# Kernel tuning notes

Measured on AMD Instinct MI355X. Metric: run time of the kernel, lower is better.

## Reference

```python
import jax, jax.numpy as jnp
import numpy as np
from jax import lax

COUNT_W, DM_W, OT_W = 3.0, 0.5, 0.3
SL1_BETA = 10.0
DM_SIGMA, DM_DS = 8.0, 4
OT_REG, OT_ITERS, OT_DS = 0.1, 50, 8
EPS = 1e-8


def _gauss_kernel(sigma):
    size = int(6 * sigma) | 1  # 49
    x = np.arange(size, dtype=np.float32) - size // 2
    xx, yy = np.meshgrid(x, x)
    k = np.exp(-(xx ** 2 + yy ** 2) / (2 * sigma ** 2))
    k = k / k.sum()
    return jnp.asarray(k, jnp.float32)[None, None], size // 2  # [1,1,S,S], pad


def _block_sum(x, d):
    # avg_pool2d(kernel=d) * d^2 == block sum
    B, C, H, W = x.shape
    return x.reshape(B, C, H // d, d, W // d, d).sum(axis=(3, 5))


def _cost_matrix(H, W):
    y, x = jnp.meshgrid(jnp.arange(H, dtype=jnp.float32),
                        jnp.arange(W, dtype=jnp.float32), indexing='ij')
    coords = jnp.stack([y.ravel(), x.ravel()], axis=1)  # [N,2]
    d = coords[:, None, :] - coords[None, :, :]
    return (d ** 2).sum(-1)  # [N,N] squared euclidean


def _dm_loss(pred, gt):
    p = _block_sum(pred, DM_DS)
    g = _block_sum(gt, DM_DS)
    kern, pad = _gauss_kernel(DM_SIGMA)
    conv = lambda z: lax.conv_general_dilated(
        z, kern, (1, 1), [(pad, pad), (pad, pad)],
        dimension_numbers=('NCHW', 'OIHW', 'NCHW'))
    ps, gs = conv(p), conv(g)
    pn = ps / jnp.maximum(ps.sum(axis=(2, 3), keepdims=True), EPS)
    gn = gs / jnp.maximum(gs.sum(axis=(2, 3), keepdims=True), EPS)
    kl = (gn * jnp.log((gn + EPS) / (pn + EPS))).sum(axis=(2, 3))
    l2 = ((pn - gn) ** 2).sum(axis=(2, 3))
    return kl.mean() + l2.mean()


def _ot_loss(pred, gt):
    p = _block_sum(pred, OT_DS)  # [B,1,h,w]
    g = _block_sum(gt, OT_DS)
    B, _, h, w = p.shape
    N = h * w
    a_raw = p.reshape(B, N)
    b_raw = g.reshape(B, N)
    a_sum = jnp.maximum(a_raw.sum(-1), EPS)
    b_sum = jnp.maximum(b_raw.sum(-1), EPS)
    a = a_raw / a_sum[:, None]
    b = b_raw / b_sum[:, None]
    C = _cost_matrix(h, w)          # [N,N]
    K = jnp.exp(-C / OT_REG)        # [N,N]

    def step(uv, _):
        u, _v = uv
        v = b / (u @ K + EPS)       # K.T @ u, batched
        u = a / (v @ K.T + EPS)     # K @ v, batched
        return (u, v), None

    (u, v), _ = lax.scan(step, (jnp.ones_like(a), jnp.ones_like(b)),
                         None, length=OT_ITERS)
    cost = jnp.einsum('bn,nm,bm->b', u, K * C, v)  # sum(P*C), P=diag(u)K diag(v)
    mask = (a_sum > 0.5) & (b_sum > 0.5)
    return jnp.where(mask, cost, 0.0).sum() / B


def reference(pred_density, gt_density, gt_counts, cell_area):
    B = pred_density.shape[0]
    # count loss (smooth L1, beta=10)
    pred_counts = jnp.maximum(pred_density.sum(axis=(1, 2, 3)) / cell_area, 0.0)
    gt_counts_f = gt_counts.astype(jnp.float32)
    diff = jnp.abs(pred_counts - gt_counts_f)
    count_loss = jnp.where(diff < SL1_BETA,
                           0.5 * diff ** 2 / SL1_BETA,
                           diff - 0.5 * SL1_BETA).mean()
    dm = _dm_loss(pred_density, gt_density)
    ot = _ot_loss(pred_density, gt_density)
    return COUNT_W * count_loss + DM_W * dm + OT_W * ot


def setup_inputs() -> dict:
    key = jax.random.key(0)
    k1, k2, k3 = jax.random.split(key, 3)
    B, H, W = 16, 512, 512
    return {
        'pred_density': jax.random.uniform(k1, (B, 1, H, W), jnp.float32),
        'gt_density': jax.random.uniform(k2, (B, 1, H, W), jnp.float32),
        'gt_counts': jax.random.randint(k3, (B,), 0, 500, jnp.int32),
        'cell_area': 1,
    }
```

## Files before the change

### kernel.cpp

```cpp
#include <hip/hip_runtime.h>
#include <math.h>

constexpr int B   = 16;
constexpr int H   = 512, W = 512;
constexpr int HW  = H * W;
constexpr int P4  = 128;
constexpr int P4N = P4 * P4;
constexpr int P8N = 64 * 64;
constexpr int NIMG = 2 * B;

constexpr float KW1 = 4.5399929762484854e-05f;
constexpr float KC2 = 4.1223072448771156e-09f;

constexpr size_t OFF_P4   = 0;
constexpr size_t OFF_CV   = OFF_P4  + (size_t)NIMG * P4N;
constexpr size_t OFF_P8   = OFF_CV  + (size_t)NIMG * P4N;
constexpr size_t OFF_PART = OFF_P8  + (size_t)NIMG * P8N;
constexpr size_t OFF_CSUM = OFF_PART + 512;

__device__ __forceinline__ float dpp_up(float x) {
    return __int_as_float(__builtin_amdgcn_update_dpp(
        0, __float_as_int(x), 0x138, 0xf, 0xf, true));
}
__device__ __forceinline__ float dpp_dn(float x) {
    return __int_as_float(__builtin_amdgcn_update_dpp(
        0, __float_as_int(x), 0x130, 0xf, 0xf, true));
}

__global__ void k_pre8(const float* __restrict__ pred, const float* __restrict__ gt,
                       float* __restrict__ ws, float* __restrict__ out, int out_size) {
    int tid = threadIdx.x, bx = blockIdx.x;
    if (bx == 0) {
        for (int i = tid; i < out_size; i += 256) out[i] = 0.f;
    }
    int gid = bx * 256 + tid;
    int img = gid >> 12;
    int rem = gid & (P8N - 1);
    int y = rem >> 6, x = rem & 63;
    const float* src = (img < B) ? (pred + (size_t)img * HW)
                                 : (gt + (size_t)(img - B) * HW);
    const float4* s4 = reinterpret_cast<const float4*>(src);
    int base = y * 8 * 128 + x * 2;
    float q00 = 0.f, q01 = 0.f, q10 = 0.f, q11 = 0.f;
#pragma unroll
    for (int r = 0; r < 8; r++) {
        float4 a0 = s4[base + r * 128];
        float4 a1 = s4[base + r * 128 + 1];
        float sa = a0.x + a0.y + a0.z + a0.w;
        float sb = a1.x + a1.y + a1.z + a1.w;
        if (r < 4) { q00 += sa; q01 += sb; } else { q10 += sa; q11 += sb; }
    }
    float* p4 = ws + OFF_P4 + (size_t)img * P4N;
    p4[(2 * y) * 128 + 2 * x]       = q00;
    p4[(2 * y) * 128 + 2 * x + 1]   = q01;
    p4[(2 * y + 1) * 128 + 2 * x]   = q10;
    p4[(2 * y + 1) * 128 + 2 * x + 1] = q11;
    float s8 = q00 + q01 + q10 + q11;
    ws[OFF_P8 + gid] = s8;
    float part = s8;
#pragma unroll
    for (int o = 32; o > 0; o >>= 1) part += __shfl_down(part, o, 64);
    __shared__ float r4[4];
    int lane = tid & 63, wid = tid >> 6;
    if (lane == 0) r4[wid] = part;
    __syncthreads();
    if (tid == 0) ws[OFF_PART + bx] = r4[0] + r4[1] + r4[2] + r4[3];
}

__global__ void __launch_bounds__(1024) k_conv(float* __restrict__ ws) {
    __shared__ float hbuf[P4N];
    __shared__ float wlds[49];
    __shared__ float rs[16];
    int img = blockIdx.x, tid = threadIdx.x;
    if (tid < 49) {
        float xx = (float)(tid - 24);
        wlds[tid] = expf(-xx * xx * (1.f / 128.f));
    }
    __syncthreads();
    float norm = 0.f;
#pragma unroll
    for (int k = 0; k < 49; k++) norm += wlds[k];
    float inv = 1.f / norm;
    const float* src = ws + OFF_P4 + (size_t)img * P4N;

#pragma unroll
    for (int g = 0; g < 2; g++) {
        int unit = g * 1024 + tid;
        int r = unit >> 4, seg = unit & 15, x0 = seg * 8;
        const float4* row4 = reinterpret_cast<const float4*>(src + (size_t)r * 128);
        float v[56];
#pragma unroll
        for (int j = 0; j < 14; j++) {
            int fx = (x0 - 24) / 4 + j;
            float4 t = (fx >= 0 && fx < 32) ? row4[fx] : make_float4(0.f, 0.f, 0.f, 0.f);
            v[4 * j] = t.x; v[4 * j + 1] = t.y; v[4 * j + 2] = t.z; v[4 * j + 3] = t.w;
        }
        float o8[8];
#pragma unroll
        for (int i = 0; i < 8; i++) o8[i] = 0.f;
#pragma unroll
        for (int k = 0; k < 49; k++) {
            float wk = wlds[k];
#pragma unroll
            for (int i = 0; i < 8; i++) o8[i] = fmaf(wk, v[i + k], o8[i]);
        }
        int sw = r & 31;
#pragma unroll
        for (int i = 0; i < 8; i++)
            hbuf[r * 128 + ((x0 + i) ^ sw)] = o8[i] * inv;
    }
    __syncthreads();

    float part = 0.f;
    float* dst = ws + OFF_CV + (size_t)img * P4N;
#pragma unroll
    for (int g = 0; g < 2; g++) {
        int unit = g * 1024 + tid;
        int c = unit & 127, rseg = unit >> 7, r0 = rseg * 8;
        float v[56];
#pragma unroll
        for (int j = 0; j < 56; j++) {
            int rr = r0 - 24 + j;
            v[j] = (rr >= 0 && rr < 128) ? hbuf[rr * 128 + (c ^ (rr & 31))] : 0.f;
        }
        float o8[8];
#pragma unroll
        for (int i = 0; i < 8; i++) o8[i] = 0.f;
#pragma unroll
        for (int k = 0; k < 49; k++) {
            float wk = wlds[k];
#pragma unroll
            for (int i = 0; i < 8; i++) o8[i] = fmaf(wk, v[i + k], o8[i]);
        }
#pragma unroll
        for (int i = 0; i < 8; i++) {
            float s = o8[i] * inv;
            dst[(size_t)(r0 + i) * 128 + c] = s;
            part += s;
        }
    }
#pragma unroll
    for (int o = 32; o > 0; o >>= 1) part += __shfl_down(part, o, 64);
    int lane = tid & 63, wid = tid >> 6;
    if (lane == 0) rs[wid] = part;
    __syncthreads();
    if (tid == 0) {
        float s = 0.f;
#pragma unroll
        for (int i = 0; i < 16; i++) s += rs[i];
        ws[OFF_CSUM + img] = s;
    }
}

__global__ void k_kll2(const float* __restrict__ ws, float* __restrict__ out) {
    int idx = blockIdx.x * 256 + threadIdx.x;
    int b = idx >> 12, rem = idx & 4095;
    const float4* cv4 = reinterpret_cast<const float4*>(ws + OFF_CV);
    float4 p = cv4[(size_t)b * 4096 + rem];
    float4 g = cv4[(size_t)(B + b) * 4096 + rem];
    float isp = 1.f / fmaxf(ws[OFF_CSUM + b], 1e-8f);
    float isg = 1.f / fmaxf(ws[OFF_CSUM + B + b], 1e-8f);
    float part = 0.f;
#pragma unroll
    for (int j = 0; j < 4; j++) {
        float pn = (j == 0 ? p.x : j == 1 ? p.y : j == 2 ? p.z : p.w) * isp;
        float gn = (j == 0 ? g.x : j == 1 ? g.y : j == 2 ? g.z : g.w) * isg;
        float d = pn - gn;
        part += gn * __logf((gn + 1e-8f) / (pn + 1e-8f)) + d * d;
    }
#pragma unroll
    for (int o = 32; o > 0; o >>= 1) part += __shfl_down(part, o, 64);
    __shared__ float r4[4];
    int lane = threadIdx.x & 63, wid = threadIdx.x >> 6;
    if (lane == 0) r4[wid] = part;
    __syncthreads();
    if (threadIdx.x == 0)
        atomicAdd(out, (0.5f / 16.f) * (r4[0] + r4[1] + r4[2] + r4[3]));
}

__device__ __forceinline__ void matvec(float* cur, const float* tgt,
                                       float* hL, float* hR, int w, int lane) {
    hL[w * 64 + lane] = cur[0];
    hR[w * 64 + lane] = cur[7];
    __syncthreads();
    float lh = (w > 0) ? hR[(w - 1) * 64 + lane] : 0.f;
    float rh = (w < 7) ? hL[(w + 1) * 64 + lane] : 0.f;
    float t[8];
    t[0] = fmaf(KW1, lh + cur[1], cur[0]);
#pragma unroll
    for (int c = 1; c < 7; c++) t[c] = fmaf(KW1, cur[c - 1] + cur[c + 1], cur[c]);
    t[7] = fmaf(KW1, cur[6] + rh, cur[7]);
#pragma unroll
    for (int c = 0; c < 8; c++) {
        float s = fmaf(KW1, dpp_up(t[c]) + dpp_dn(t[c]), t[c]) + 1e-8f;
        cur[c] = tgt[c] * __builtin_amdgcn_rcpf(s);
    }
}

__global__ void __launch_bounds__(512) k_ot(const float* __restrict__ ws,
                                            const int* __restrict__ gtc,
                                            const int* __restrict__ carea,
                                            float* __restrict__ out) {
    __shared__ float smem[2 * 64 * 65];
    __shared__ float rsum[8];
    int b = blockIdx.x, tid = threadIdx.x;
    int lane = tid & 63;
    int w = tid >> 6;
    float* hL0 = smem;            float* hR0 = smem + 512;
    float* hL1 = smem + 1024;     float* hR1 = smem + 1536;

    const float* PART = ws + OFF_PART;
    float rawA = 0.f, rawB = 0.f;
#pragma unroll
    for (int j = 0; j < 16; j++) {
        rawA += PART[b * 16 + j];
        rawB += PART[(B + b) * 16 + j];
    }
    float asum = fmaxf(rawA, 1e-8f), bsum = fmaxf(rawB, 1e-8f);
    float ai = 1.f / asum, bi = 1.f / bsum;

    const float* ap = ws + OFF_P8 + (size_t)b * P8N;
    const float* bp = ws + OFF_P8 + (size_t)(B + b) * P8N;
    for (int i = tid; i < P8N; i += 512) {
        int r = i >> 6, c = i & 63;
        smem[r * 65 + c] = ap[i];
        smem[64 * 65 + r * 65 + c] = bp[i];
    }
    __syncthreads();
    float ar[8], br[8], cur[8], vv[8];
    int gc = w * 8;
#pragma unroll
    for (int c = 0; c < 8; c++) {
        ar[c] = smem[lane * 65 + gc + c] * ai;
        br[c] = smem[64 * 65 + lane * 65 + gc + c] * bi;
        cur[c] = 1.f;
    }
    __syncthreads();

    for (int it = 0; it < 50; it++) {
        matvec(cur, br, hL0, hR0, w, lane);
        if (it == 49) {
#pragma unroll
            for (int c = 0; c < 8; c++) vv[c] = cur[c];
        }
        matvec(cur, ar, hL1, hR1, w, lane);
    }

    hL0[w * 64 + lane] = vv[0];
    hR0[w * 64 + lane] = vv[7];
    __syncthreads();
    float V[10];
    V[0] = (w > 0) ? hR0[(w - 1) * 64 + lane] : 0.f;
    V[9] = (w < 7) ? hL0[(w + 1) * 64 + lane] : 0.f;
#pragma unroll
    for (int c = 0; c < 8; c++) V[c + 1] = vv[c];
    float U[10], D[10];
#pragma unroll
    for (int i = 0; i < 10; i++) { U[i] = dpp_up(V[i]); D[i] = dpp_dn(V[i]); }
    float part = 0.f;
#pragma unroll
    for (int c = 0; c < 8; c++) {
        float s = KW1 * (V[c] + V[c + 2] + U[c + 1] + D[c + 1])
                + KC2 * (U[c] + D[c] + U[c + 2] + D[c + 2]);
        part += cur[c] * s;
    }
#pragma unroll
    for (int o = 32; o > 0; o >>= 1) part += __shfl_down(part, o, 64);
    if (lane == 0) rsum[w] = part;
    __syncthreads();
    if (tid == 0) {
        float c = 0.f;
#pragma unroll
        for (int i = 0; i < 8; i++) c += rsum[i];
        float ot = (asum > 0.5f && bsum > 0.5f) ? c : 0.f;
        int cv = carea[0];
        float ca = (cv >= 1 && cv < 16777216) ? (float)cv : __int_as_float(cv);
        float pc = fmaxf(rawA / ca, 0.f);
        float d = fabsf(pc - (float)gtc[b]);
        float cl = (d < 10.f) ? (0.05f * d * d) : (d - 5.f);
        atomicAdd(out, 0.3f * ot * (1.f / 16.f) + 3.f * cl * (1.f / 16.f));
    }
}

extern "C" void kernel_launch(void* const* d_in, const int* in_sizes, int n_in,
                              void* d_out, int out_size, void* d_ws, size_t ws_size,
                              hipStream_t stream) {
    const float* pred = (const float*)d_in[0];
    const float* gt   = (const float*)d_in[1];
    const int* gtc    = (const int*)d_in[2];
    const int* ca     = (const int*)d_in[3];
    float* out = (float*)d_out;
    float* ws  = (float*)d_ws;

    k_pre8<<<512, 256, 0, stream>>>(pred, gt, ws, out, out_size);
    k_conv<<<32, 1024, 0, stream>>>(ws);
    k_kll2<<<256, 256, 0, stream>>>(ws, out);
    k_ot<<<16, 512, 0, stream>>>(ws, gtc, ca, out);
}
```

Before: 137.5 us.

## Merge conv and OT Sinkhorn into one launch running on disjoint blocks

Folds the separable Gaussian conv kernel and the OT Sinkhorn kernel into a single 48-block launch: 32 blocks do the conv at 512 threads and 16 blocks run Sinkhorn. The two stages run concurrently and one launch is dropped. The Sinkhorn layout changes from column strips to row strips read straight from global memory. Each iteration now computes v with halo rows, so it needs one barrier per iteration instead of two, using double-buffered halos. The conv blocks now have half the threads, each doing twice the work, which may lengthen the conv phase.

After: 123.8 us. 10.0% less time.

```diff
diff --git a/kernel.cpp b/kernel.cpp
--- a/kernel.cpp
+++ b/kernel.cpp
@@ -51,9 +51,9 @@
         if (r < 4) { q00 += sa; q01 += sb; } else { q10 += sa; q11 += sb; }
     }
     float* p4 = ws + OFF_P4 + (size_t)img * P4N;
-    p4[(2 * y) * 128 + 2 * x]       = q00;
-    p4[(2 * y) * 128 + 2 * x + 1]   = q01;
-    p4[(2 * y + 1) * 128 + 2 * x]   = q10;
+    p4[(2 * y) * 128 + 2 * x]         = q00;
+    p4[(2 * y) * 128 + 2 * x + 1]     = q01;
+    p4[(2 * y + 1) * 128 + 2 * x]     = q10;
     p4[(2 * y + 1) * 128 + 2 * x + 1] = q11;
     float s8 = q00 + q01 + q10 + q11;
     ws[OFF_P8 + gid] = s8;
@@ -67,88 +67,188 @@
     if (tid == 0) ws[OFF_PART + bx] = r4[0] + r4[1] + r4[2] + r4[3];
 }
 
-__global__ void __launch_bounds__(1024) k_conv(float* __restrict__ ws) {
-    __shared__ float hbuf[P4N];
-    __shared__ float wlds[49];
-    __shared__ float rs[16];
-    int img = blockIdx.x, tid = threadIdx.x;
-    if (tid < 49) {
-        float xx = (float)(tid - 24);
-        wlds[tid] = expf(-xx * xx * (1.f / 128.f));
-    }
-    __syncthreads();
-    float norm = 0.f;
-#pragma unroll
-    for (int k = 0; k < 49; k++) norm += wlds[k];
-    float inv = 1.f / norm;
-    const float* src = ws + OFF_P4 + (size_t)img * P4N;
-
-#pragma unroll
-    for (int g = 0; g < 2; g++) {
-        int unit = g * 1024 + tid;
-        int r = unit >> 4, seg = unit & 15, x0 = seg * 8;
-        const float4* row4 = reinterpret_cast<const float4*>(src + (size_t)r * 128);
-        float v[56];
-#pragma unroll
-        for (int j = 0; j < 14; j++) {
-            int fx = (x0 - 24) / 4 + j;
-            float4 t = (fx >= 0 && fx < 32) ? row4[fx] : make_float4(0.f, 0.f, 0.f, 0.f);
-            v[4 * j] = t.x; v[4 * j + 1] = t.y; v[4 * j + 2] = t.z; v[4 * j + 3] = t.w;
-        }
-        float o8[8];
-#pragma unroll
-        for (int i = 0; i < 8; i++) o8[i] = 0.f;
-#pragma unroll
-        for (int k = 0; k < 49; k++) {
-            float wk = wlds[k];
-#pragma unroll
-            for (int i = 0; i < 8; i++) o8[i] = fmaf(wk, v[i + k], o8[i]);
-        }
-        int sw = r & 31;
-#pragma unroll
-        for (int i = 0; i < 8; i++)
-            hbuf[r * 128 + ((x0 + i) ^ sw)] = o8[i] * inv;
-    }
-    __syncthreads();
-
-    float part = 0.f;
-    float* dst = ws + OFF_CV + (size_t)img * P4N;
-#pragma unroll
-    for (int g = 0; g < 2; g++) {
-        int unit = g * 1024 + tid;
-        int c = unit & 127, rseg = unit >> 7, r0 = rseg * 8;
-        float v[56];
-#pragma unroll
-        for (int j = 0; j < 56; j++) {
-            int rr = r0 - 24 + j;
-            v[j] = (rr >= 0 && rr < 128) ? hbuf[rr * 128 + (c ^ (rr & 31))] : 0.f;
-        }
-        float o8[8];
-#pragma unroll
-        for (int i = 0; i < 8; i++) o8[i] = 0.f;
-#pragma unroll
-        for (int k = 0; k < 49; k++) {
-            float wk = wlds[k];
-#pragma unroll
-            for (int i = 0; i < 8; i++) o8[i] = fmaf(wk, v[i + k], o8[i]);
-        }
-#pragma unroll
-        for (int i = 0; i < 8; i++) {
-            float s = o8[i] * inv;
-            dst[(size_t)(r0 + i) * 128 + c] = s;
-            part += s;
-        }
-    }
-#pragma unroll
-    for (int o = 32; o > 0; o >>= 1) part += __shfl_down(part, o, 64);
-    int lane = tid & 63, wid = tid >> 6;
-    if (lane == 0) rs[wid] = part;
-    __syncthreads();
-    if (tid == 0) {
-        float s = 0.f;
-#pragma unroll
-        for (int i = 0; i < 16; i++) s += rs[i];
-        ws[OFF_CSUM + img] = s;
+__global__ void __launch_bounds__(512) k_mega(float* __restrict__ ws,
+                                              const int* __restrict__ gtc,
+                                              const int* __restrict__ carea,
+                                              float* __restrict__ out) {
+    __shared__ float sh[P4N + 80];
+    int tid = threadIdx.x;
+    int lane = tid & 63, w = tid >> 6;
+
+    if (blockIdx.x < 32) {
+        int img = blockIdx.x;
+        float* hbuf = sh;
+        float* wlds = sh + P4N;
+        float* rs   = sh + P4N + 56;
+        if (tid < 49) {
+            float xx = (float)(tid - 24);
+            wlds[tid] = expf(-xx * xx * (1.f / 128.f));
+        }
+        __syncthreads();
+        float norm = 0.f;
+#pragma unroll
+        for (int k = 0; k < 49; k++) norm += wlds[k];
+        float inv = 1.f / norm;
+        const float* src = ws + OFF_P4 + (size_t)img * P4N;
+
+#pragma unroll
+        for (int g = 0; g < 4; g++) {
+            int unit = g * 512 + tid;
+            int r = unit >> 4, seg = unit & 15, x0 = seg * 8;
+            const float4* row4 = reinterpret_cast<const float4*>(src + (size_t)r * 128);
+            float v[56];
+#pragma unroll
+            for (int j = 0; j < 14; j++) {
+                int fx = (x0 - 24) / 4 + j;
+                float4 t = (fx >= 0 && fx < 32) ? row4[fx] : make_float4(0.f, 0.f, 0.f, 0.f);
+                v[4 * j] = t.x; v[4 * j + 1] = t.y; v[4 * j + 2] = t.z; v[4 * j + 3] = t.w;
+            }
+            float o8[8];
+#pragma unroll
+            for (int i = 0; i < 8; i++) o8[i] = 0.f;
+#pragma unroll
+            for (int k = 0; k < 49; k++) {
+                float wk = wlds[k];
+#pragma unroll
+                for (int i = 0; i < 8; i++) o8[i] = fmaf(wk, v[i + k], o8[i]);
+            }
+            int sw = r & 31;
+#pragma unroll
+            for (int i = 0; i < 8; i++)
+                hbuf[r * 128 + ((x0 + i) ^ sw)] = o8[i] * inv;
+        }
+        __syncthreads();
+
+        float part = 0.f;
+        float* dst = ws + OFF_CV + (size_t)img * P4N;
+#pragma unroll
+        for (int g = 0; g < 4; g++) {
+            int unit = g * 512 + tid;
+            int c = unit & 127, rseg = unit >> 7, r0 = rseg * 8;
+            float v[56];
+#pragma unroll
+            for (int j = 0; j < 56; j++) {
+                int rr = r0 - 24 + j;
+                v[j] = (rr >= 0 && rr < 128) ? hbuf[rr * 128 + (c ^ (rr & 31))] : 0.f;
+            }
+            float o8[8];
+#pragma unroll
+            for (int i = 0; i < 8; i++) o8[i] = 0.f;
+#pragma unroll
+            for (int k = 0; k < 49; k++) {
+                float wk = wlds[k];
+#pragma unroll
+                for (int i = 0; i < 8; i++) o8[i] = fmaf(wk, v[i + k], o8[i]);
+            }
+#pragma unroll
+            for (int i = 0; i < 8; i++) {
+                float s = o8[i] * inv;
+                dst[(size_t)(r0 + i) * 128 + c] = s;
+                part += s;
+            }
+        }
+#pragma unroll
+        for (int o = 32; o > 0; o >>= 1) part += __shfl_down(part, o, 64);
+        if (lane == 0) rs[w] = part;
+        __syncthreads();
+        if (tid == 0) {
+            float s = 0.f;
+#pragma unroll
+            for (int i = 0; i < 8; i++) s += rs[i];
+            ws[OFF_CSUM + img] = s;
+        }
+    } else {
+        int b = blockIdx.x - 32;
+        int r0 = w << 3;
+        float* H0 = sh;
+        float* H1 = sh + 2048;
+        float* rsum = sh + 4096;
+
+        const float* PART = ws + OFF_PART;
+        float rawA = 0.f, rawB = 0.f;
+#pragma unroll
+        for (int j = 0; j < 16; j++) {
+            rawA += PART[b * 16 + j];
+            rawB += PART[(B + b) * 16 + j];
+        }
+        float asum = fmaxf(rawA, 1e-8f), bsum = fmaxf(rawB, 1e-8f);
+        float ai = 1.f / asum, bi = 1.f / bsum;
+        const float* ap = ws + OFF_P8 + (size_t)b * P8N;
+        const float* bp = ws + OFF_P8 + (size_t)(B + b) * P8N;
+
+        float ar[8], br10[10], cur[8], vr[10];
+#pragma unroll
+        for (int k = 0; k < 8; k++) {
+            ar[k] = ap[(r0 + k) * 64 + lane] * ai;
+            cur[k] = 1.f;
+        }
+#pragma unroll
+        for (int i = 0; i < 10; i++) {
+            int rr = r0 - 1 + i;
+            br10[i] = (rr >= 0 && rr < 64) ? bp[rr * 64 + lane] * bi : 0.f;
+        }
+
+        for (int it = 0; it < 50; it++) {
+            float* Hp = (it & 1) ? H1 : H0;
+            Hp[(0 * 8 + w) * 64 + lane] = cur[0];
+            Hp[(1 * 8 + w) * 64 + lane] = cur[1];
+            Hp[(2 * 8 + w) * 64 + lane] = cur[6];
+            Hp[(3 * 8 + w) * 64 + lane] = cur[7];
+            __syncthreads();
+            float uext[12];
+            uext[0]  = w ? Hp[(2 * 8 + w - 1) * 64 + lane] : 0.f;
+            uext[1]  = w ? Hp[(3 * 8 + w - 1) * 64 + lane] : 0.f;
+#pragma unroll
+            for (int k = 0; k < 8; k++) uext[2 + k] = cur[k];
+            uext[10] = (w < 7) ? Hp[(0 * 8 + w + 1) * 64 + lane] : 0.f;
+            uext[11] = (w < 7) ? Hp[(1 * 8 + w + 1) * 64 + lane] : 0.f;
+
+            float tr[10];
+#pragma unroll
+            for (int i = 0; i < 10; i++)
+                tr[i] = fmaf(KW1, uext[i] + uext[i + 2], uext[i + 1]);
+#pragma unroll
+            for (int i = 0; i < 10; i++) {
+                float s = fmaf(KW1, dpp_up(tr[i]) + dpp_dn(tr[i]), tr[i]) + 1e-8f;
+                vr[i] = br10[i] * __builtin_amdgcn_rcpf(s);
+            }
+            float t2[8];
+#pragma unroll
+            for (int k = 0; k < 8; k++)
+                t2[k] = fmaf(KW1, vr[k] + vr[k + 2], vr[k + 1]);
+#pragma unroll
+            for (int k = 0; k < 8; k++) {
+                float s = fmaf(KW1, dpp_up(t2[k]) + dpp_dn(t2[k]), t2[k]) + 1e-8f;
+                cur[k] = ar[k] * __builtin_amdgcn_rcpf(s);
+            }
+        }
+
+        float dL[10], dR[10];
+#pragma unroll
+        for (int i = 0; i < 10; i++) { dL[i] = dpp_up(vr[i]); dR[i] = dpp_dn(vr[i]); }
+        float part = 0.f;
+#pragma unroll
+        for (int k = 0; k < 8; k++) {
+            float s = KW1 * (vr[k] + vr[k + 2] + dL[k + 1] + dR[k + 1])
+                    + KC2 * (dL[k] + dR[k] + dL[k + 2] + dR[k + 2]);
+            part = fmaf(cur[k], s, part);
+        }
+#pragma unroll
+        for (int o = 32; o > 0; o >>= 1) part += __shfl_down(part, o, 64);
+        if (lane == 0) rsum[w] = part;
+        __syncthreads();
+        if (tid == 0) {
+            float c = 0.f;
+#pragma unroll
+            for (int i = 0; i < 8; i++) c += rsum[i];
+            float ot = (asum > 0.5f && bsum > 0.5f) ? c : 0.f;
+            int cv = carea[0];
+            float ca = (cv >= 1 && cv < 16777216) ? (float)cv : __int_as_float(cv);
+            float pc = fmaxf(rawA / ca, 0.f);
+            float d = fabsf(pc - (float)gtc[b]);
+            float cl = (d < 10.f) ? (0.05f * d * d) : (d - 5.f);
+            atomicAdd(out, 0.3f * ot * (1.f / 16.f) + 3.f * cl * (1.f / 16.f));
+        }
     }
 }
 
@@ -178,110 +278,6 @@
         atomicAdd(out, (0.5f / 16.f) * (r4[0] + r4[1] + r4[2] + r4[3]));
 }
 
-__device__ __forceinline__ void matvec(float* cur, const float* tgt,
-                                       float* hL, float* hR, int w, int lane) {
-    hL[w * 64 + lane] = cur[0];
-    hR[w * 64 + lane] = cur[7];
-    __syncthreads();
-    float lh = (w > 0) ? hR[(w - 1) * 64 + lane] : 0.f;
-    float rh = (w < 7) ? hL[(w + 1) * 64 + lane] : 0.f;
-    float t[8];
-    t[0] = fmaf(KW1, lh + cur[1], cur[0]);
-#pragma unroll
-    for (int c = 1; c < 7; c++) t[c] = fmaf(KW1, cur[c - 1] + cur[c + 1], cur[c]);
-    t[7] = fmaf(KW1, cur[6] + rh, cur[7]);
-#pragma unroll
-    for (int c = 0; c < 8; c++) {
-        float s = fmaf(KW1, dpp_up(t[c]) + dpp_dn(t[c]), t[c]) + 1e-8f;
-        cur[c] = tgt[c] * __builtin_amdgcn_rcpf(s);
-    }
-}
-
-__global__ void __launch_bounds__(512) k_ot(const float* __restrict__ ws,
-                                            const int* __restrict__ gtc,
-                                            const int* __restrict__ carea,
-                                            float* __restrict__ out) {
-    __shared__ float smem[2 * 64 * 65];
-    __shared__ float rsum[8];
-    int b = blockIdx.x, tid = threadIdx.x;
-    int lane = tid & 63;
-    int w = tid >> 6;
-    float* hL0 = smem;            float* hR0 = smem + 512;
-    float* hL1 = smem + 1024;     float* hR1 = smem + 1536;
-
-    const float* PART = ws + OFF_PART;
-    float rawA = 0.f, rawB = 0.f;
-#pragma unroll
-    for (int j = 0; j < 16; j++) {
-        rawA += PART[b * 16 + j];
-        rawB += PART[(B + b) * 16 + j];
-    }
-    float asum = fmaxf(rawA, 1e-8f), bsum = fmaxf(rawB, 1e-8f);
-    float ai = 1.f / asum, bi = 1.f / bsum;
-
-    const float* ap = ws + OFF_P8 + (size_t)b * P8N;
-    const float* bp = ws + OFF_P8 + (size_t)(B + b) * P8N;
-    for (int i = tid; i < P8N; i += 512) {
-        int r = i >> 6, c = i & 63;
-        smem[r * 65 + c] = ap[i];
-        smem[64 * 65 + r * 65 + c] = bp[i];
-    }
-    __syncthreads();
-    float ar[8], br[8], cur[8], vv[8];
-    int gc = w * 8;
-#pragma unroll
-    for (int c = 0; c < 8; c++) {
-        ar[c] = smem[lane * 65 + gc + c] * ai;
-        br[c] = smem[64 * 65 + lane * 65 + gc + c] * bi;
-        cur[c] = 1.f;
-    }
-    __syncthreads();
-
-    for (int it = 0; it < 50; it++) {
-        matvec(cur, br, hL0, hR0, w, lane);
-        if (it == 49) {
-#pragma unroll
-            for (int c = 0; c < 8; c++) vv[c] = cur[c];
-        }
-        matvec(cur, ar, hL1, hR1, w, lane);
-    }
-
-    hL0[w * 64 + lane] = vv[0];
-    hR0[w * 64 + lane] = vv[7];
-    __syncthreads();
-    float V[10];
-    V[0] = (w > 0) ? hR0[(w - 1) * 64 + lane] : 0.f;
-    V[9] = (w < 7) ? hL0[(w + 1) * 64 + lane] : 0.f;
-#pragma unroll
-    for (int c = 0; c < 8; c++) V[c + 1] = vv[c];
-    float U[10], D[10];
-#pragma unroll
-    for (int i = 0; i < 10; i++) { U[i] = dpp_up(V[i]); D[i] = dpp_dn(V[i]); }
-    float part = 0.f;
-#pragma unroll
-    for (int c = 0; c < 8; c++) {
-        float s = KW1 * (V[c] + V[c + 2] + U[c + 1] + D[c + 1])
-                + KC2 * (U[c] + D[c] + U[c + 2] + D[c + 2]);
-        part += cur[c] * s;
-    }
-#pragma unroll
-    for (int o = 32; o > 0; o >>= 1) part += __shfl_down(part, o, 64);
-    if (lane == 0) rsum[w] = part;
-    __syncthreads();
-    if (tid == 0) {
-        float c = 0.f;
-#pragma unroll
-        for (int i = 0; i < 8; i++) c += rsum[i];
-        float ot = (asum > 0.5f && bsum > 0.5f) ? c : 0.f;
-        int cv = carea[0];
-        float ca = (cv >= 1 && cv < 16777216) ? (float)cv : __int_as_float(cv);
-        float pc = fmaxf(rawA / ca, 0.f);
-        float d = fabsf(pc - (float)gtc[b]);
-        float cl = (d < 10.f) ? (0.05f * d * d) : (d - 5.f);
-        atomicAdd(out, 0.3f * ot * (1.f / 16.f) + 3.f * cl * (1.f / 16.f));
-    }
-}
-
 extern "C" void kernel_launch(void* const* d_in, const int* in_sizes, int n_in,
                               void* d_out, int out_size, void* d_ws, size_t ws_size,
                               hipStream_t stream) {
@@ -293,7 +289,6 @@
     float* ws  = (float*)d_ws;
 
     k_pre8<<<512, 256, 0, stream>>>(pred, gt, ws, out, out_size);
-    k_conv<<<32, 1024, 0, stream>>>(ws);
+    k_mega<<<48, 512, 0, stream>>>(ws, gtc, ca, out);
     k_kll2<<<256, 256, 0, stream>>>(ws, out);
-    k_ot<<<16, 512, 0, stream>>>(ws, gtc, ca, out);
-}
+}
```
